# Optimization experiments

Hardware: AMD Instinct MI355X
Metric: run time of the kernel (lower is better)

## Reference

```python
import jax, jax.numpy as jnp
import numpy as np

N, E = 50000, 800000
F_IN, HID, OUT, H = 128, 32, 4, 8
NEG_SLOPE = 0.2


def gat_conv(x, src, dst, W, a_src, a_dst, b):
    """PyG GATConv (concat=True, eval mode). x: [N,Fin]; src/dst: [E'] (self-loops included).
    W: [Fin, Hh*C]; a_src/a_dst: [Hh, C]; b: [Hh*C]."""
    n = x.shape[0]
    Hh, C = a_src.shape
    h = (x @ W).reshape(n, Hh, C)                      # [N,H,C]
    alpha_src = jnp.einsum('nhc,hc->nh', h, a_src)     # [N,H]
    alpha_dst = jnp.einsum('nhc,hc->nh', h, a_dst)     # [N,H]
    alpha = jax.nn.leaky_relu(alpha_src[src] + alpha_dst[dst], NEG_SLOPE)  # [E',H]
    # segment softmax over incoming edges of each dst node
    amax = jax.ops.segment_max(alpha, dst, num_segments=n)  # [N,H]
    ex = jnp.exp(alpha - amax[dst])
    denom = jax.ops.segment_sum(ex, dst, num_segments=n)    # [N,H]
    w = ex / (denom[dst] + 1e-16)                            # [E',H]
    msg = h[src] * w[:, :, None]                             # [E',H,C]
    out = jax.ops.segment_sum(msg, dst, num_segments=n)     # [N,H,C]
    return out.reshape(n, Hh * C) + b


def setup_inputs() -> dict:
    key = jax.random.key(0)
    ks = jax.random.split(key, 9)
    x = jax.random.normal(ks[0], (N, F_IN), jnp.float32)
    # random edge list without self loops (PyG GATConv removes then re-adds self loops)
    rng = np.random.default_rng(0)
    s = rng.integers(0, N, size=E)
    d = rng.integers(0, N, size=E)
    d = np.where(d == s, (d + 1) % N, d)
    edge_index = jnp.asarray(np.stack([s, d]), dtype=jnp.int32)
    g = lambda k, shape, fan: jax.random.normal(k, shape, jnp.float32) * (1.0 / np.sqrt(fan))
    W1 = g(ks[1], (F_IN, H * HID), F_IN)
    a_src1 = g(ks[2], (H, HID), HID)
    a_dst1 = g(ks[3], (H, HID), HID)
    b1 = jnp.zeros((H * HID,), jnp.float32)
    W2 = g(ks[4], (H * HID, H * OUT), H * HID)
    a_src2 = g(ks[5], (H, OUT), OUT)
    a_dst2 = g(ks[6], (H, OUT), OUT)
    b2 = jnp.zeros((H * OUT,), jnp.float32)
    return {"x": x, "edge_index": edge_index, "W1": W1, "a_src1": a_src1,
            "a_dst1": a_dst1, "b1": b1, "W2": W2, "a_src2": a_src2,
            "a_dst2": a_dst2, "b2": b2}


def reference(x, edge_index, W1, a_src1, a_dst1, b1, W2, a_src2, a_dst2, b2):
    n = x.shape[0]
    loops = jnp.arange(n, dtype=edge_index.dtype)
    src = jnp.concatenate([edge_index[0], loops])
    dst = jnp.concatenate([edge_index[1], loops])
    # layer 1 (dropout_edge / dropout are no-ops in eval mode)
    h = gat_conv(x, src, dst, W1, a_src1, a_dst1, b1)
    h = jax.nn.leaky_relu(h, NEG_SLOPE)
    # final layer (concat=True per the original code) -> [N, OUT*H]
    out = gat_conv(h, src, dst, W2, a_src2, a_dst2, b2)
    return out
```

## Files before the change

### kernel.cpp

```cpp
#include <hip/hip_runtime.h>
#include <hip/hip_bf16.h>
#include <cstdint>
#include <cstddef>


__device__ __forceinline__ float lrelu(float a) { return a > 0.f ? a : 0.2f * a; }

__device__ __forceinline__ unsigned short f2bf(float f) {
  unsigned u = __float_as_uint(f);
  unsigned r = (u + 0x7fff + ((u >> 16) & 1)) >> 16;
  return (unsigned short)r;
}
__device__ __forceinline__ float bf_lo(unsigned q) { return __uint_as_float(q << 16); }
__device__ __forceinline__ float bf_hi(unsigned q) { return __uint_as_float(q & 0xffff0000u); }

typedef __attribute__((ext_vector_type(8))) short bf16x8;
typedef __attribute__((ext_vector_type(4))) float f32x4;

#define ROWCAP 64


__global__ __launch_bounds__(256) void k_scatter(const int* __restrict__ srce,
                                                 const int* __restrict__ dste, int E, int n,
                                                 int* __restrict__ cursor,
                                                 int* __restrict__ srcs,
                                                 const float* __restrict__ W1,
                                                 unsigned short* __restrict__ W1T,
                                                 const float* __restrict__ W2,
                                                 unsigned short* __restrict__ W2T,
                                                 const float* __restrict__ as1,
                                                 const float* __restrict__ ad1,
                                                 const float* __restrict__ as2,
                                                 const float* __restrict__ ad2,
                                                 unsigned short* __restrict__ Wa1T,
                                                 unsigned short* __restrict__ Wa2T) {
  int t = blockIdx.x * 256 + threadIdx.x;
  if (t < E + n) {
    int s, d;
    if (t < E) { s = srce[t]; d = dste[t]; } else { s = d = t - E; }
    int pos = atomicAdd(&cursor[d], 1);
    srcs[(d << 6) + pos] = s;
  }
  if (t < 32768) {
    int k = t >> 8;
    int nn = t & 255;
    W1T[nn * 128 + k] = f2bf(W1[k * 256 + nn]);
  }
  if (t < 8192) {
    int k = t >> 5;
    int nn = t & 31;
    W2T[nn * 256 + k] = f2bf(W2[k * 32 + nn]);
  }
  if (t < 2048) {
    int j = t >> 7;
    int k = t & 127;
    const float* av = (j < 8) ? &as1[j * 32] : &ad1[(j - 8) * 32];
    const float* wv = &W1[k * 256 + (j & 7) * 32];
    float s = 0.f;
#pragma unroll
    for (int c = 0; c < 32; c++) s += wv[c] * av[c];
    Wa1T[j * 128 + k] = f2bf(s);
  }
  if (t < 4096) {
    int j = t >> 8;
    int k = t & 255;
    const float* av = (j < 8) ? &as2[j * 4] : &ad2[(j - 8) * 4];
    const float* wv = &W2[k * 32 + (j & 7) * 4];
    float s = 0.f;
#pragma unroll
    for (int c = 0; c < 4; c++) s += wv[c] * av[c];
    Wa2T[j * 256 + k] = f2bf(s);
  }
}


__global__ __launch_bounds__(256) void gemm1_mfma(const float* __restrict__ X,
                                                  const unsigned short* __restrict__ WT,
                                                  const unsigned short* __restrict__ WaT,
                                                  unsigned short* __restrict__ h1,
                                                  float* __restrict__ a_s1,
                                                  float* __restrict__ a_d1,
                                                  int M) {
  __shared__ unsigned short As[64 * 136];
  __shared__ unsigned short Bs[256 * 72];
  __shared__ unsigned short Was[16 * 72];
  const int row0 = blockIdx.x * 64;
  const int tid = threadIdx.x;
  const int wv = tid >> 6, lane = tid & 63;
  const int quad = lane >> 4, l15 = lane & 15;
  const int colw = wv * 64;

#pragma unroll
  for (int i = 0; i < 8; i++) {
    int j = tid + 256 * i;
    int r = j >> 5;
    int c4 = (j & 31) * 4;
    float4 v = make_float4(0.f, 0.f, 0.f, 0.f);
    if (row0 + r < M) v = *(const float4*)&X[(size_t)(row0 + r) * 128 + c4];
    uint2 p;
    p.x = (unsigned)f2bf(v.x) | ((unsigned)f2bf(v.y) << 16);
    p.y = (unsigned)f2bf(v.z) | ((unsigned)f2bf(v.w) << 16);
    *(uint2*)&As[r * 136 + c4] = p;
  }

  f32x4 acc[16];
#pragma unroll
  for (int i = 0; i < 16; i++) acc[i] = (f32x4)0.f;
  f32x4 acca = (f32x4)0.f;

  for (int kc = 0; kc < 128; kc += 64) {
    __syncthreads();
#pragma unroll
    for (int i = 0; i < 8; i++) {
      int j = tid + 256 * i;
      int nn = j >> 3;
      int kg = (j & 7) * 8;
      *(uint4*)&Bs[nn * 72 + kg] = *(const uint4*)&WT[nn * 128 + kc + kg];
    }
    if (tid < 128) {
      int j = tid >> 3;
      int kg = (tid & 7) * 8;
      *(uint4*)&Was[j * 72 + kg] = *(const uint4*)&WaT[j * 128 + kc + kg];
    }
    __syncthreads();
#pragma unroll
    for (int ks = 0; ks < 64; ks += 32) {
      bf16x8 af[4], bfr[4];
#pragma unroll
      for (int mi = 0; mi < 4; mi++)
        af[mi] = *(const bf16x8*)&As[(mi * 16 + l15) * 136 + kc + ks + quad * 8];
#pragma unroll
      for (int ni = 0; ni < 4; ni++)
        bfr[ni] = *(const bf16x8*)&Bs[(colw + ni * 16 + l15) * 72 + ks + quad * 8];
#pragma unroll
      for (int mi = 0; mi < 4; mi++)
#pragma unroll
        for (int ni = 0; ni < 4; ni++)
          acc[mi * 4 + ni] = __builtin_amdgcn_mfma_f32_16x16x32_bf16(
              af[mi], bfr[ni], acc[mi * 4 + ni], 0, 0, 0);
      bf16x8 afa = *(const bf16x8*)&As[(wv * 16 + l15) * 136 + kc + ks + quad * 8];
      bf16x8 bfa = *(const bf16x8*)&Was[l15 * 72 + ks + quad * 8];
      acca = __builtin_amdgcn_mfma_f32_16x16x32_bf16(afa, bfa, acca, 0, 0, 0);
    }
  }

#pragma unroll
  for (int mi = 0; mi < 4; mi++) {
#pragma unroll
    for (int r = 0; r < 4; r++) {
      int m = row0 + mi * 16 + quad * 4 + r;
      if (m < M) {
#pragma unroll
        for (int ni = 0; ni < 4; ni++)
          h1[(size_t)m * 256 + colw + ni * 16 + l15] = f2bf(acc[mi * 4 + ni][r]);
      }
    }
  }
#pragma unroll
  for (int r = 0; r < 4; r++) {
    int m = row0 + wv * 16 + quad * 4 + r;
    if (m < M) {
      if (l15 < 8) a_s1[m * 8 + l15] = acca[r];
      else         a_d1[m * 8 + (l15 - 8)] = acca[r];
    }
  }
}


__global__ __launch_bounds__(256) void gemm2_mfma(const unsigned short* __restrict__ Xb,
                                                  const unsigned short* __restrict__ W2T,
                                                  const unsigned short* __restrict__ WaT,
                                                  unsigned short* __restrict__ h2,
                                                  float* __restrict__ a_s2,
                                                  float* __restrict__ a_d2, int M) {
  __shared__ unsigned short As[64 * 264];
  __shared__ unsigned short Bs[32 * 264];
  __shared__ unsigned short Was[16 * 264];
  const int row0 = blockIdx.x * 64;
  const int tid = threadIdx.x;
  const int wv = tid >> 6, lane = tid & 63;
  const int quad = lane >> 4, l15 = lane & 15;

#pragma unroll
  for (int i = 0; i < 8; i++) {
    int j = tid + 256 * i;
    int r = j >> 5;
    int c8 = (j & 31) * 8;
    uint4 v = make_uint4(0, 0, 0, 0);
    if (row0 + r < M) v = *(const uint4*)&Xb[(size_t)(row0 + r) * 256 + c8];
    *(uint4*)&As[r * 264 + c8] = v;
  }
#pragma unroll
  for (int i = 0; i < 4; i++) {
    int j = tid + 256 * i;
    int nn = j >> 5;
    int kg = (j & 31) * 8;
    *(uint4*)&Bs[nn * 264 + kg] = *(const uint4*)&W2T[nn * 256 + kg];
  }
#pragma unroll
  for (int i = 0; i < 2; i++) {
    int j = tid + 256 * i;
    int nn = j >> 5;
    int kg = (j & 31) * 8;
    *(uint4*)&Was[nn * 264 + kg] = *(const uint4*)&WaT[nn * 256 + kg];
  }
  __syncthreads();

  f32x4 acc[2];
  acc[0] = (f32x4)0.f;
  acc[1] = (f32x4)0.f;
  f32x4 acca = (f32x4)0.f;
  const int mr = wv * 16;
#pragma unroll
  for (int ks = 0; ks < 256; ks += 32) {
    bf16x8 af = *(const bf16x8*)&As[(mr + l15) * 264 + ks + quad * 8];
    bf16x8 b0 = *(const bf16x8*)&Bs[(l15) * 264 + ks + quad * 8];
    bf16x8 b1 = *(const bf16x8*)&Bs[(16 + l15) * 264 + ks + quad * 8];
    bf16x8 ba = *(const bf16x8*)&Was[(l15) * 264 + ks + quad * 8];
    acc[0] = __builtin_amdgcn_mfma_f32_16x16x32_bf16(af, b0, acc[0], 0, 0, 0);
    acc[1] = __builtin_amdgcn_mfma_f32_16x16x32_bf16(af, b1, acc[1], 0, 0, 0);
    acca   = __builtin_amdgcn_mfma_f32_16x16x32_bf16(af, ba, acca, 0, 0, 0);
  }

#pragma unroll
  for (int r = 0; r < 4; r++) {
    int m = row0 + mr + quad * 4 + r;
    if (m < M) {
      h2[(size_t)m * 32 + l15]      = f2bf(acc[0][r]);
      h2[(size_t)m * 32 + 16 + l15] = f2bf(acc[1][r]);
      if (l15 < 8) a_s2[m * 8 + l15] = acca[r];
      else         a_d2[m * 8 + (l15 - 8)] = acca[r];
    }
  }
}


__global__ __launch_bounds__(256) void gat_agg_l1(const unsigned short* __restrict__ h,
                                                  const float* __restrict__ asrc,
                                                  const float* __restrict__ adst,
                                                  const int* __restrict__ rowcnt,
                                                  const int* __restrict__ srcs,
                                                  const float* __restrict__ bias,
                                                  unsigned short* __restrict__ out, int n) {
  int wave = threadIdx.x >> 6;
  int lane = threadIdx.x & 63;
  int d = blockIdx.x * 4 + wave;
  if (d >= n) return;
  d = __builtin_amdgcn_readfirstlane(d);
  const int cnt = __builtin_amdgcn_readfirstlane(rowcnt[d]);
  const int* __restrict__ row = srcs + (d << 6);
  const int myhead = lane >> 3;
  float ad = adst[d * 8 + myhead];

  float denom = 0.f;
  float4 acc0 = make_float4(0.f, 0.f, 0.f, 0.f);
  float4 acc1 = make_float4(0.f, 0.f, 0.f, 0.f);
#define ACCA(ff, qq)                                        \
    acc0.x = fmaf(ff, bf_lo(qq.x), acc0.x);                 \
    acc0.y = fmaf(ff, bf_hi(qq.x), acc0.y);                 \
    acc0.z = fmaf(ff, bf_lo(qq.y), acc0.z);                 \
    acc0.w = fmaf(ff, bf_hi(qq.y), acc0.w);
#define ACCB(ff, qq)                                        \
    acc1.x = fmaf(ff, bf_lo(qq.x), acc1.x);                 \
    acc1.y = fmaf(ff, bf_hi(qq.x), acc1.y);                 \
    acc1.z = fmaf(ff, bf_lo(qq.y), acc1.z);                 \
    acc1.w = fmaf(ff, bf_hi(qq.y), acc1.w);

  for (int e = 0; e < cnt; e += 12) {
    int s[12];
#pragma unroll
    for (int j = 0; j < 12; j++) {
      int ee = e + j;
      s[j] = __builtin_amdgcn_readfirstlane(row[ee < cnt ? ee : cnt - 1]);
    }
    uint2 q[12];
#pragma unroll
    for (int j = 0; j < 12; j++)
      q[j] = *(const uint2*)&h[(size_t)s[j] * 256 + lane * 4];
    float av[12];
#pragma unroll
    for (int j = 0; j < 12; j++) av[j] = asrc[s[j] * 8 + myhead];
#pragma unroll
    for (int j = 0; j < 12; j += 2) {
      float w0 = (e + j     < cnt) ? __expf(lrelu(av[j]     + ad)) : 0.f;
      float w1 = (e + j + 1 < cnt) ? __expf(lrelu(av[j + 1] + ad)) : 0.f;
      denom += w0 + w1;
      ACCA(w0, q[j])
      ACCB(w1, q[j + 1])
    }
  }
#undef ACCA
#undef ACCB
  float4 acc;
  acc.x = acc0.x + acc1.x;
  acc.y = acc0.y + acc1.y;
  acc.z = acc0.z + acc1.z;
  acc.w = acc0.w + acc1.w;
  float inv = 1.f / (denom + 1e-16f);
  int f = lane * 4;
  float4 bv = *(const float4*)&bias[f];
  float rx = lrelu(acc.x * inv + bv.x);
  float ry = lrelu(acc.y * inv + bv.y);
  float rz = lrelu(acc.z * inv + bv.z);
  float rw = lrelu(acc.w * inv + bv.w);
  uint2 p;
  p.x = (unsigned)f2bf(rx) | ((unsigned)f2bf(ry) << 16);
  p.y = (unsigned)f2bf(rz) | ((unsigned)f2bf(rw) << 16);
  *(uint2*)&out[(size_t)d * 256 + f] = p;
}

__global__ __launch_bounds__(256) void gat_agg_l2(const unsigned short* __restrict__ h,
                                                  const float* __restrict__ asrc,
                                                  const float* __restrict__ adst,
                                                  const int* __restrict__ rowcnt,
                                                  const int* __restrict__ srcs,
                                                  const float* __restrict__ bias,
                                                  float* __restrict__ out, int n) {
  int wave = threadIdx.x >> 6;
  int lane = threadIdx.x & 63;
  int d = blockIdx.x * 4 + wave;
  if (d >= n) return;
  int begin = d << 6;
  int end = begin + rowcnt[d];
  int hh = lane & 7;
  int eg = lane >> 3;
  float ad = adst[d * 8 + hh];

  float denom = 0.f;
  float4 acc = make_float4(0.f, 0.f, 0.f, 0.f);
  for (int base = begin; base < end; base += 32) {
    int eA = base + eg;
    int eB = base + 8 + eg;
    int eC = base + 16 + eg;
    int eD = base + 24 + eg;
    bool vA = eA < end, vB = eB < end, vC = eC < end, vD = eD < end;
    int sA = srcs[vA ? eA : begin];
    int sB = srcs[vB ? eB : begin];
    int sC = srcs[vC ? eC : begin];
    int sD = srcs[vD ? eD : begin];
    float aA = asrc[sA * 8 + hh];
    float aB = asrc[sB * 8 + hh];
    float aC = asrc[sC * 8 + hh];
    float aD = asrc[sD * 8 + hh];
    uint2 qA = *(const uint2*)&h[(size_t)sA * 32 + hh * 4];
    uint2 qB = *(const uint2*)&h[(size_t)sB * 32 + hh * 4];
    uint2 qC = *(const uint2*)&h[(size_t)sC * 32 + hh * 4];
    uint2 qD = *(const uint2*)&h[(size_t)sD * 32 + hh * 4];
    float wA = vA ? __expf(lrelu(aA + ad)) : 0.f;
    float wB = vB ? __expf(lrelu(aB + ad)) : 0.f;
    float wC = vC ? __expf(lrelu(aC + ad)) : 0.f;
    float wD = vD ? __expf(lrelu(aD + ad)) : 0.f;
    denom += (wA + wB) + (wC + wD);
    acc.x = fmaf(wA, bf_lo(qA.x), acc.x); acc.y = fmaf(wA, bf_hi(qA.x), acc.y);
    acc.z = fmaf(wA, bf_lo(qA.y), acc.z); acc.w = fmaf(wA, bf_hi(qA.y), acc.w);
    acc.x = fmaf(wB, bf_lo(qB.x), acc.x); acc.y = fmaf(wB, bf_hi(qB.x), acc.y);
    acc.z = fmaf(wB, bf_lo(qB.y), acc.z); acc.w = fmaf(wB, bf_hi(qB.y), acc.w);
    acc.x = fmaf(wC, bf_lo(qC.x), acc.x); acc.y = fmaf(wC, bf_hi(qC.x), acc.y);
    acc.z = fmaf(wC, bf_lo(qC.y), acc.z); acc.w = fmaf(wC, bf_hi(qC.y), acc.w);
    acc.x = fmaf(wD, bf_lo(qD.x), acc.x); acc.y = fmaf(wD, bf_hi(qD.x), acc.y);
    acc.z = fmaf(wD, bf_lo(qD.y), acc.z); acc.w = fmaf(wD, bf_hi(qD.y), acc.w);
  }
#pragma unroll
  for (int mask = 8; mask <= 32; mask <<= 1) {
    denom += __shfl_xor(denom, mask);
    acc.x += __shfl_xor(acc.x, mask);
    acc.y += __shfl_xor(acc.y, mask);
    acc.z += __shfl_xor(acc.z, mask);
    acc.w += __shfl_xor(acc.w, mask);
  }
  if (lane < 8) {
    float inv = 1.f / (denom + 1e-16f);
    int f = lane * 4;
    float4 bv = *(const float4*)&bias[f];
    float4 r;
    r.x = acc.x * inv + bv.x;
    r.y = acc.y * inv + bv.y;
    r.z = acc.z * inv + bv.z;
    r.w = acc.w * inv + bv.w;
    *(float4*)&out[(size_t)d * 32 + f] = r;
  }
}


extern "C" void kernel_launch(void* const* d_in, const int* in_sizes, int n_in,
                              void* d_out, int out_size, void* d_ws, size_t ws_size,
                              hipStream_t stream) {
  const float* x   = (const float*)d_in[0];
  const int*   ei  = (const int*)d_in[1];
  const float* W1  = (const float*)d_in[2];
  const float* as1 = (const float*)d_in[3];
  const float* ad1 = (const float*)d_in[4];
  const float* b1  = (const float*)d_in[5];
  const float* W2  = (const float*)d_in[6];
  const float* as2 = (const float*)d_in[7];
  const float* ad2 = (const float*)d_in[8];
  const float* b2  = (const float*)d_in[9];
  float* out = (float*)d_out;

  const int E = in_sizes[1] / 2;
  const int n = in_sizes[0] / 128;
  const int* srce = ei;
  const int* dste = ei + E;

  char* ws = (char*)d_ws;
  size_t off = 0;
  auto alloc = [&](size_t bytes) -> void* {
    void* p = ws + off;
    off = (off + bytes + 255) & ~(size_t)255;
    return p;
  };
  int* cursor   = (int*)alloc((size_t)n * 4);
  int* srcs     = (int*)alloc((size_t)n * ROWCAP * 4);
  unsigned short* h1  = (unsigned short*)alloc((size_t)n * 256 * 2);
  unsigned short* w1t = (unsigned short*)alloc((size_t)256 * 128 * 2);
  unsigned short* w2t = (unsigned short*)alloc((size_t)32 * 256 * 2);
  unsigned short* wa1t = (unsigned short*)alloc((size_t)16 * 128 * 2);
  unsigned short* wa2t = (unsigned short*)alloc((size_t)16 * 256 * 2);
  float* a_s1   = (float*)alloc((size_t)n * 8 * 4);
  float* a_d1   = (float*)alloc((size_t)n * 8 * 4);
  unsigned short* x2 = (unsigned short*)alloc((size_t)n * 256 * 2);
  unsigned short* h2 = (unsigned short*)alloc((size_t)n * 32 * 2);
  float* a_s2   = (float*)alloc((size_t)n * 8 * 4);
  float* a_d2   = (float*)alloc((size_t)n * 8 * 4);

  const int tot = E + n;
  hipMemsetAsync(cursor, 0, (size_t)n * 4, stream);
  k_scatter<<<(tot + 255) / 256, 256, 0, stream>>>(srce, dste, E, n, cursor, srcs,
                                                   W1, w1t, W2, w2t,
                                                   as1, ad1, as2, ad2, wa1t, wa2t);

  gemm1_mfma<<<(n + 63) / 64, 256, 0, stream>>>(x, w1t, wa1t, h1, a_s1, a_d1, n);
  gat_agg_l1<<<(n + 3) / 4, 256, 0, stream>>>(h1, a_s1, a_d1, cursor, srcs, b1, x2, n);

  gemm2_mfma<<<(n + 63) / 64, 256, 0, stream>>>(x2, w2t, wa2t, h2, a_s2, a_d2, n);
  gat_agg_l2<<<(n + 3) / 4, 256, 0, stream>>>(h2, a_s2, a_d2, cursor, srcs, b2, out, n);
}
```

Baseline: 251.2 us.

## Fuse edge bucketing into GEMM1 and pad per-node cursors to separate lines

Moves the edge scatter (atomic per-destination cursor plus source list fill) out of the prep kernel and into the tail of gemm1 as a grid-stride loop, leaving a small 128-block k_prep for the weight transposes. Each node's cursor now sits on its own 64-byte slot (stride 16 ints), which is meant to cut atomic contention and false sharing. The aim is to hide the atomic-heavy scatter behind GEMM work and shrink a large launch. In exchange the cursor memset grows 16x and gemm1 blocks carry extra latency-bound atomic work.

```diff
diff --git a/kernel.cpp b/kernel.cpp
--- a/kernel.cpp
+++ b/kernel.cpp
@@ -18,29 +18,20 @@
 typedef __attribute__((ext_vector_type(4))) float f32x4;
 
 #define ROWCAP 64
-
-
-__global__ __launch_bounds__(256) void k_scatter(const int* __restrict__ srce,
-                                                 const int* __restrict__ dste, int E, int n,
-                                                 int* __restrict__ cursor,
-                                                 int* __restrict__ srcs,
-                                                 const float* __restrict__ W1,
-                                                 unsigned short* __restrict__ W1T,
-                                                 const float* __restrict__ W2,
-                                                 unsigned short* __restrict__ W2T,
-                                                 const float* __restrict__ as1,
-                                                 const float* __restrict__ ad1,
-                                                 const float* __restrict__ as2,
-                                                 const float* __restrict__ ad2,
-                                                 unsigned short* __restrict__ Wa1T,
-                                                 unsigned short* __restrict__ Wa2T) {
+#define CSTRIDE 16
+
+
+__global__ __launch_bounds__(256) void k_prep(const float* __restrict__ W1,
+                                              unsigned short* __restrict__ W1T,
+                                              const float* __restrict__ W2,
+                                              unsigned short* __restrict__ W2T,
+                                              const float* __restrict__ as1,
+                                              const float* __restrict__ ad1,
+                                              const float* __restrict__ as2,
+                                              const float* __restrict__ ad2,
+                                              unsigned short* __restrict__ Wa1T,
+                                              unsigned short* __restrict__ Wa2T) {
   int t = blockIdx.x * 256 + threadIdx.x;
-  if (t < E + n) {
-    int s, d;
-    if (t < E) { s = srce[t]; d = dste[t]; } else { s = d = t - E; }
-    int pos = atomicAdd(&cursor[d], 1);
-    srcs[(d << 6) + pos] = s;
-  }
   if (t < 32768) {
     int k = t >> 8;
     int nn = t & 255;
@@ -80,7 +71,11 @@
                                                   unsigned short* __restrict__ h1,
                                                   float* __restrict__ a_s1,
                                                   float* __restrict__ a_d1,
-                                                  int M) {
+                                                  int M,
+                                                  const int* __restrict__ srce,
+                                                  const int* __restrict__ dste, int E,
+                                                  int* __restrict__ cursor,
+                                                  int* __restrict__ srcs) {
   __shared__ unsigned short As[64 * 136];
   __shared__ unsigned short Bs[256 * 72];
   __shared__ unsigned short Was[16 * 72];
@@ -163,6 +158,15 @@
       if (l15 < 8) a_s1[m * 8 + l15] = acca[r];
       else         a_d1[m * 8 + (l15 - 8)] = acca[r];
     }
+  }
+
+  const int En = E + M;
+  const int stride = gridDim.x * 256;
+  for (int t = blockIdx.x * 256 + tid; t < En; t += stride) {
+    int s, dd;
+    if (t < E) { s = srce[t]; dd = dste[t]; } else { s = dd = t - E; }
+    int pos = atomicAdd(&cursor[dd << 4], 1);
+    srcs[(dd << 6) + pos] = s;
   }
 }
 
@@ -247,7 +251,7 @@
   int d = blockIdx.x * 4 + wave;
   if (d >= n) return;
   d = __builtin_amdgcn_readfirstlane(d);
-  const int cnt = __builtin_amdgcn_readfirstlane(rowcnt[d]);
+  const int cnt = __builtin_amdgcn_readfirstlane(rowcnt[d << 4]);
   const int* __restrict__ row = srcs + (d << 6);
   const int myhead = lane >> 3;
   float ad = adst[d * 8 + myhead];
@@ -321,7 +325,7 @@
   int d = blockIdx.x * 4 + wave;
   if (d >= n) return;
   int begin = d << 6;
-  int end = begin + rowcnt[d];
+  int end = begin + rowcnt[d << 4];
   int hh = lane & 7;
   int eg = lane >> 3;
   float ad = adst[d * 8 + hh];
@@ -409,7 +413,7 @@
     off = (off + bytes + 255) & ~(size_t)255;
     return p;
   };
-  int* cursor   = (int*)alloc((size_t)n * 4);
+  int* cursor   = (int*)alloc((size_t)n * CSTRIDE * 4);
   int* srcs     = (int*)alloc((size_t)n * ROWCAP * 4);
   unsigned short* h1  = (unsigned short*)alloc((size_t)n * 256 * 2);
   unsigned short* w1t = (unsigned short*)alloc((size_t)256 * 128 * 2);
@@ -423,13 +427,11 @@
   float* a_s2   = (float*)alloc((size_t)n * 8 * 4);
   float* a_d2   = (float*)alloc((size_t)n * 8 * 4);
 
-  const int tot = E + n;
-  hipMemsetAsync(cursor, 0, (size_t)n * 4, stream);
-  k_scatter<<<(tot + 255) / 256, 256, 0, stream>>>(srce, dste, E, n, cursor, srcs,
-                                                   W1, w1t, W2, w2t,
-                                                   as1, ad1, as2, ad2, wa1t, wa2t);
-
-  gemm1_mfma<<<(n + 63) / 64, 256, 0, stream>>>(x, w1t, wa1t, h1, a_s1, a_d1, n);
+  hipMemsetAsync(cursor, 0, (size_t)n * CSTRIDE * 4, stream);
+  k_prep<<<128, 256, 0, stream>>>(W1, w1t, W2, w2t, as1, ad1, as2, ad2, wa1t, wa2t);
+
+  gemm1_mfma<<<(n + 63) / 64, 256, 0, stream>>>(x, w1t, wa1t, h1, a_s1, a_d1, n,
+                                                srce, dste, E, cursor, srcs);
   gat_agg_l1<<<(n + 3) / 4, 256, 0, stream>>>(h1, a_s1, a_d1, cursor, srcs, b1, x2, n);
 
   gemm2_mfma<<<(n + 63) / 64, 256, 0, stream>>>(x2, w2t, wa2t, h2, a_s2, a_d2, n);
```

New measurement: 272.4 us. +8.4%, slower.
